# Kernel tuning notes

Hardware: AMD Instinct MI355X
Metric: run time of the kernel (lower is better)

The kernel has to match this reference:

```python
import jax, jax.numpy as jnp
import numpy as np

C_IN, C = 16, 32
N = 150000
SHAPE = (480, 360, 32)
SLOPE = 0.01  # LeakyReLU default
EPS = 1e-5    # BatchNorm1d default

# offset index into the canonical 27-neighbor table, ordered (dz, dy, dx)
P133 = tuple(9 + (dy + 1) * 3 + (dx + 1) for dy in (-1, 0, 1) for dx in (-1, 0, 1))   # kernel (1,3,3)
P313 = tuple((dz + 1) * 9 + 3 + (dx + 1) for dz in (-1, 0, 1) for dx in (-1, 0, 1))   # kernel (3,1,3)
P311 = tuple((dz + 1) * 9 + 4 for dz in (-1, 0, 1))                                   # kernel (3,1,1)
P131 = tuple(9 + (dy + 1) * 3 + 1 for dy in (-1, 0, 1))                               # kernel (1,3,1)
P113 = (12, 13, 14)                                                                   # kernel (1,1,3)


def setup_inputs() -> dict:
    rng = np.random.default_rng(0)
    # unique active voxel linear coords, sorted for searchsorted lookup
    lin = np.sort(rng.choice(SHAPE[0] * SHAPE[1] * SHAPE[2], size=N, replace=False))
    z, yx = np.divmod(lin, SHAPE[1] * SHAPE[2])
    y, x = np.divmod(yx, SHAPE[2])
    coords = np.stack([z, y, x], 1)  # [N,3]
    offs = np.array([[dz, dy, dx] for dz in (-1, 0, 1) for dy in (-1, 0, 1) for dx in (-1, 0, 1)])
    nc = coords[None] + offs[:, None]  # [27,N,3]
    valid = (nc >= 0).all(-1) & (nc[..., 0] < SHAPE[0]) & (nc[..., 1] < SHAPE[1]) & (nc[..., 2] < SHAPE[2])
    nlin = nc[..., 0] * SHAPE[1] * SHAPE[2] + nc[..., 1] * SHAPE[2] + nc[..., 2]
    pos = np.clip(np.searchsorted(lin, nlin), 0, N - 1)
    found = valid & (lin[pos] == nlin)
    nbr = np.where(found, pos, -1).astype(np.int32)  # [27,N], spconv indice pairs

    key = jax.random.key(0)
    ks = jax.random.split(key, 9)
    w = lambda k, kk, ci, co: jax.random.normal(k, (kk, ci, co), jnp.float32) * (1.0 / np.sqrt(kk * ci))
    bn_params = jnp.stack([
        jnp.stack([1.0 + 0.1 * jax.random.normal(jax.random.fold_in(ks[8], 4 * i + 0), (C,)),
                   0.1 * jax.random.normal(jax.random.fold_in(ks[8], 4 * i + 1), (C,)),
                   0.1 * jax.random.normal(jax.random.fold_in(ks[8], 4 * i + 2), (C,)),
                   0.5 + jax.random.uniform(jax.random.fold_in(ks[8], 4 * i + 3), (C,))])
        for i in range(7)
    ])  # [7,4,C]: gamma, beta, running_mean, running_var
    return {
        "x_feat": jax.random.normal(ks[0], (N, C_IN), jnp.float32),
        "nbr": jnp.asarray(nbr),
        "W1": w(ks[1], 9, C_IN, C), "W12": w(ks[2], 9, C, C),
        "W2": w(ks[3], 9, C_IN, C), "W3": w(ks[4], 9, C, C),
        "Wr1": w(ks[5], 3, C, C), "Wr2": w(ks[6], 3, C, C), "Wr3": w(ks[7], 3, C, C),
        "bn_params": bn_params,
    }


def _subm(feat, nbr, W, offs):
    """Submanifold sparse conv: gather -> masked GEMM -> same active set."""
    idx = nbr[jnp.asarray(offs)]              # [K,N]
    g = feat[jnp.clip(idx, 0)]                # [K,N,Cin]
    g = jnp.where((idx >= 0)[..., None], g, jnp.zeros((), feat.dtype))
    return jnp.einsum('knc,kcd->nd', g, W)    # [N,Cout]


def _bn(f, p):  # eval-mode BatchNorm1d
    gamma, beta, mean, var = p[0], p[1], p[2], p[3]
    return gamma * (f - mean) * jax.lax.rsqrt(var + EPS) + beta


def _lrelu(f):
    return jnp.where(f >= 0, f, SLOPE * f)


def reference(x_feat, nbr, W1, W12, W2, W3, Wr1, Wr2, Wr3, bn_params):
    # ResContextBlock (downCntx): act then BN, per source
    s = _bn(_lrelu(_subm(x_feat, nbr, W1, P133)), bn_params[0])
    s = _bn(_lrelu(_subm(s, nbr, W12, P313)), bn_params[1])
    r = _bn(_lrelu(_subm(x_feat, nbr, W2, P313)), bn_params[2])
    r = _bn(_lrelu(_subm(r, nbr, W3, P133)), bn_params[3])
    y = r + s
    # ReconBlock: three axial convs -> BN -> sigmoid, summed, gating multiply
    a = jax.nn.sigmoid(_bn(_subm(y, nbr, Wr1, P311), bn_params[4]))
    b = jax.nn.sigmoid(_bn(_subm(y, nbr, Wr2, P131), bn_params[5]))
    c = jax.nn.sigmoid(_bn(_subm(y, nbr, Wr3, P113), bn_params[6]))
    return (a + b + c) * y
```

## Files before the change

### kernel.cpp

```cpp
#include <hip/hip_runtime.h>
#include <cstdint>
#include <cstddef>


#define SLOPE 0.01f
#define BN_EPS 1e-5f

typedef __attribute__((ext_vector_type(8))) short bf16x8;
typedef __attribute__((ext_vector_type(4))) float f32x4;

__device__ __forceinline__ float bflo(uint32_t w) {
    union { uint32_t i; float f; } v; v.i = w << 16; return v.f;
}
__device__ __forceinline__ float bfhi(uint32_t w) {
    union { uint32_t i; float f; } v; v.i = w & 0xffff0000u; return v.f;
}
__device__ __forceinline__ float bf2f(uint16_t u) {
    union { uint32_t i; float f; } v; v.i = ((uint32_t)u) << 16; return v.f;
}
__device__ __forceinline__ uint16_t f2bf(float f) {
    union { float f; uint32_t i; } v; v.f = f;
    uint32_t x = v.i;
    return (uint16_t)((x + 0x7fffu + ((x >> 16) & 1u)) >> 16);
}

struct Taps9 { int t[9]; };
struct WSrcs { const void* p[8]; };

#define WFS     18432
#define WF_END  (5 * WFS)
#define BN_CNT  896

__device__ __forceinline__ int detect_f32_inline(const uint16_t* x16)
{
    int lane = threadIdx.x & 63;
    float a = bf2f(x16[4 * lane]);
    float b = bf2f(x16[4 * lane + 2]);
    int bad = (!(a > -16.f && a < 16.f)) || (!(b > -16.f && b < 16.f));
    return __ballot(bad) != 0ull;
}

__device__ __forceinline__ float readw(const void* p, int j, int f32)
{
    return f32 ? ((const float*)p)[j] : bf2f(((const uint16_t*)p)[j]);
}

__global__ void prep_all(const uint16_t* __restrict__ xprobe, WSrcs srcs,
                         uint16_t* __restrict__ Wf, float* __restrict__ bnf)
{
    int f32 = detect_f32_inline(xprobe);
    int i = blockIdx.x * 256 + threadIdx.x;
    if (i < WF_END) {
        int s = i / WFS, r = i - s * WFS;
        int t = r >> 11, T = (r >> 10) & 1;
        int co = (r >> 5) & 31, k = r & 31;
        uint16_t outv;
        if (s == 0 || s == 2) {
            int c = k >> 1, p = k & 1;
            float w = readw(srcs.p[s == 0 ? 0 : 2], (t * 16 + c) * 32 + co, f32);
            uint16_t h = f2bf(w);
            outv = (T == 0) ? h : (p == 0 ? f2bf(w - bf2f(h)) : (uint16_t)0);
        } else {
            float w;
            if (s == 4) {
                int g = t / 3, kk = t - g * 3;
                const void* bnp = srcs.p[7];
                float ga = readw(bnp, (4 + g) * 128 + co, f32);
                float va = readw(bnp, (4 + g) * 128 + 96 + co, f32);
                float scl = ga * rsqrtf(va + BN_EPS);
                w = readw(srcs.p[4 + g], (kk * 32 + k) * 32 + co, f32) * scl;
            } else {
                w = readw(srcs.p[s == 1 ? 1 : 3], (t * 32 + k) * 32 + co, f32);
            }
            uint16_t h = f2bf(w);
            outv = (T == 0) ? h : f2bf(w - bf2f(h));
        }
        Wf[i] = outv;
    } else if (i < WF_END + BN_CNT) {
        bnf[i - WF_END] = readw(srcs.p[7], i - WF_END, f32);
    }
}

__global__ void canon_x3(const void* __restrict__ xsrc,
                         uint32_t* __restrict__ xi, int total)
{
    int f32 = detect_f32_inline((const uint16_t*)xsrc);
    for (int i = blockIdx.x * blockDim.x + threadIdx.x; i < total;
         i += gridDim.x * blockDim.x) {
        float v = f32 ? ((const float*)xsrc)[i]
                      : bf2f(((const uint16_t*)xsrc)[i]);
        int row = i >> 4, c = i & 15;
        uint16_t h = f2bf(v);
        uint16_t l = f2bf(v - bf2f(h));
        xi[(size_t)row * 16 + c] = (uint32_t)h | ((uint32_t)l << 16);
    }
}

struct ConvJob {
    const uint16_t* feat;
    const uint16_t* Wf;
    const float*    bn;
    const uint16_t* addsrc;
    uint16_t*       out;
    Taps9 taps;
};

#define MFMA_BF16(A, B, C) __builtin_amdgcn_mfma_f32_16x16x32_bf16(A, B, C, 0, 0, 0)

__launch_bounds__(256, 3)
__global__ void conv_mfma5(ConvJob j0, ConvJob j1,
                           const int* __restrict__ nbr, int N)
{
    const ConvJob J = (blockIdx.y == 1) ? j1 : j0;
    const int tid = threadIdx.x;
    const int n0  = blockIdx.x * 128;
    const int lane = tid & 63;
    const int m = lane & 15, q = lane >> 4;
    const int vt0 = (tid >> 6) * 32;
    const bf16x8 Z8 = {0, 0, 0, 0, 0, 0, 0, 0};

    int rows[9][2];
#pragma unroll
    for (int t = 0; t < 9; ++t)
#pragma unroll
        for (int vt = 0; vt < 2; ++vt) {
            int n = n0 + vt0 + vt * 16 + m;
            rows[t][vt] = (n < N) ? nbr[(size_t)J.taps.t[t] * N + n] : -1;
        }
    __builtin_amdgcn_sched_barrier(0);

    bf16x8 A[9][2];
#pragma unroll
    for (int t = 0; t < 9; ++t)
#pragma unroll
        for (int vt = 0; vt < 2; ++vt) {
            int row = rows[t][vt];
            A[t][vt] = Z8;
            if (row >= 0)
                A[t][vt] = *(const bf16x8*)(J.feat + (size_t)row * 32 + q * 8);
        }
    __builtin_amdgcn_sched_barrier(0);

    f32x4 acc[2][2];
#pragma unroll
    for (int vt = 0; vt < 2; ++vt)
#pragma unroll
        for (int ot = 0; ot < 2; ++ot) acc[vt][ot] = {0.f, 0.f, 0.f, 0.f};

#pragma unroll
    for (int t = 0; t < 9; ++t) {
        const uint16_t* wb = J.Wf + t * 2048 + m * 32 + q * 8;
        bf16x8 B00 = *(const bf16x8*)(wb);
        bf16x8 B10 = *(const bf16x8*)(wb + 1024);
        bf16x8 B01 = *(const bf16x8*)(wb + 512);
        bf16x8 B11 = *(const bf16x8*)(wb + 1536);
#pragma unroll
        for (int vt = 0; vt < 2; ++vt) {
            acc[vt][0] = MFMA_BF16(A[t][vt], B00, acc[vt][0]);
            acc[vt][0] = MFMA_BF16(A[t][vt], B10, acc[vt][0]);
            acc[vt][1] = MFMA_BF16(A[t][vt], B01, acc[vt][1]);
            acc[vt][1] = MFMA_BF16(A[t][vt], B11, acc[vt][1]);
        }
    }

#pragma unroll
    for (int ot = 0; ot < 2; ++ot) {
        int ch = ot * 16 + m;
        float ga = J.bn[ch], be = J.bn[32 + ch];
        float mu = J.bn[64 + ch], va = J.bn[96 + ch];
        float s = ga * rsqrtf(va + BN_EPS);
        float b = be - mu * s;
#pragma unroll
        for (int vt = 0; vt < 2; ++vt)
#pragma unroll
            for (int r = 0; r < 4; ++r) {
                int vox = n0 + vt0 + vt * 16 + q * 4 + r;
                if (vox >= N) continue;
                float xv = acc[vt][ot][r];
                xv = (xv >= 0.f) ? xv : SLOPE * xv;
                float o = xv * s + b;
                if (J.addsrc) o += bf2f(J.addsrc[(size_t)vox * 32 + ch]);
                J.out[(size_t)vox * 32 + ch] = f2bf(o);
            }
    }
}

__launch_bounds__(256, 3)
__global__ void recon_mfma5(const uint16_t* __restrict__ y16,
                            const uint16_t* __restrict__ xprobe,
                            const int* __restrict__ nbr,
                            const uint16_t* __restrict__ Wf4,
                            const float* __restrict__ bnf,
                            void* __restrict__ out_, int N)
{
    const int out_f32 = detect_f32_inline(xprobe);
    const int tid = threadIdx.x;
    const int n0  = blockIdx.x * 128;
    const int lane = tid & 63;
    const int m = lane & 15, q = lane >> 4;
    const int vt0 = (tid >> 6) * 32;
    const bf16x8 Z8 = {0, 0, 0, 0, 0, 0, 0, 0};

    const int ut[7] = {4, 22, 10, 16, 12, 14, 13};
    int rows[7][2];
#pragma unroll
    for (int t = 0; t < 7; ++t)
#pragma unroll
        for (int vt = 0; vt < 2; ++vt) {
            int n = n0 + vt0 + vt * 16 + m;
            rows[t][vt] = (n < N) ? nbr[(size_t)ut[t] * N + n] : -1;
        }
    __builtin_amdgcn_sched_barrier(0);

    bf16x8 A[7][2];
#pragma unroll
    for (int t = 0; t < 7; ++t)
#pragma unroll
        for (int vt = 0; vt < 2; ++vt) {
            int row = rows[t][vt];
            A[t][vt] = Z8;
            if (row >= 0)
                A[t][vt] = *(const bf16x8*)(y16 + (size_t)row * 32 + q * 8);
        }
    __builtin_amdgcn_sched_barrier(0);

    f32x4 a[3][2][2];
#pragma unroll
    for (int g = 0; g < 3; ++g)
#pragma unroll
        for (int vt = 0; vt < 2; ++vt)
#pragma unroll
            for (int ot = 0; ot < 2; ++ot) a[g][vt][ot] = {0.f, 0.f, 0.f, 0.f};

#pragma unroll
    for (int e = 0; e < 3; ++e)
#pragma unroll
        for (int s2 = 0; s2 < 2; ++s2) {
            int slot = 2 * e + s2;
            int t = e * 3 + s2 * 2;
            const uint16_t* wb = Wf4 + t * 2048 + m * 32 + q * 8;
            bf16x8 B00 = *(const bf16x8*)(wb);
            bf16x8 B10 = *(const bf16x8*)(wb + 1024);
            bf16x8 B01 = *(const bf16x8*)(wb + 512);
            bf16x8 B11 = *(const bf16x8*)(wb + 1536);
#pragma unroll
            for (int vt = 0; vt < 2; ++vt) {
                a[e][vt][0] = MFMA_BF16(A[slot][vt], B00, a[e][vt][0]);
                a[e][vt][0] = MFMA_BF16(A[slot][vt], B10, a[e][vt][0]);
                a[e][vt][1] = MFMA_BF16(A[slot][vt], B01, a[e][vt][1]);
                a[e][vt][1] = MFMA_BF16(A[slot][vt], B11, a[e][vt][1]);
            }
        }
#pragma unroll
    for (int g = 0; g < 3; ++g) {
        const uint16_t* wb = Wf4 + (g * 3 + 1) * 2048 + m * 32 + q * 8;
        bf16x8 B00 = *(const bf16x8*)(wb);
        bf16x8 B10 = *(const bf16x8*)(wb + 1024);
        bf16x8 B01 = *(const bf16x8*)(wb + 512);
        bf16x8 B11 = *(const bf16x8*)(wb + 1536);
#pragma unroll
        for (int vt = 0; vt < 2; ++vt) {
            a[g][vt][0] = MFMA_BF16(A[6][vt], B00, a[g][vt][0]);
            a[g][vt][0] = MFMA_BF16(A[6][vt], B10, a[g][vt][0]);
            a[g][vt][1] = MFMA_BF16(A[6][vt], B01, a[g][vt][1]);
            a[g][vt][1] = MFMA_BF16(A[6][vt], B11, a[g][vt][1]);
        }
    }

#pragma unroll
    for (int ot = 0; ot < 2; ++ot) {
        int ch = ot * 16 + m;
        float sh[3];
#pragma unroll
        for (int g = 0; g < 3; ++g) {
            const float* p = bnf + (size_t)(4 + g) * 128;
            float scl = p[ch] * rsqrtf(p[96 + ch] + BN_EPS);
            sh[g] = p[32 + ch] - p[64 + ch] * scl;
        }
#pragma unroll
        for (int vt = 0; vt < 2; ++vt)
#pragma unroll
            for (int r = 0; r < 4; ++r) {
                int vox = n0 + vt0 + vt * 16 + q * 4 + r;
                if (vox >= N) continue;
                float g0 = 1.f / (1.f + __expf(-(a[0][vt][ot][r] + sh[0])));
                float g1 = 1.f / (1.f + __expf(-(a[1][vt][ot][r] + sh[1])));
                float g2 = 1.f / (1.f + __expf(-(a[2][vt][ot][r] + sh[2])));
                float o = (g0 + g1 + g2) * bf2f(y16[(size_t)vox * 32 + ch]);
                if (out_f32)
                    ((float*)out_)[(size_t)vox * 32 + ch] = o;
                else
                    ((uint16_t*)out_)[(size_t)vox * 32 + ch] = f2bf(o);
            }
    }
}

#define WC_W1   0
#define WC_W12  4608
#define WC_W2   13824
#define WC_W3   18432
#define WC_WR1  27648
#define WC_WR2  30720
#define WC_WR3  33792
#define WC_BNP  36864
#define WC_END  37760

__global__ void canon_weights_fb(WSrcs srcs, float* __restrict__ Wc,
                                 const uint16_t* __restrict__ xprobe)
{
    int f32 = detect_f32_inline(xprobe);
    const int offs[9] = {WC_W1, WC_W12, WC_W2, WC_W3, WC_WR1, WC_WR2,
                         WC_WR3, WC_BNP, WC_END};
    int i = blockIdx.x * 256 + threadIdx.x;
    if (i >= WC_END) return;
    int t = 0;
#pragma unroll
    for (int k = 1; k < 8; ++k) if (i >= offs[k]) t = k;
    Wc[i] = readw(srcs.p[t], i - offs[t], f32);
}

__global__ void canon_x_bf(const void* __restrict__ xsrc,
                           uint16_t* __restrict__ xc, int n)
{
    int f32 = detect_f32_inline((const uint16_t*)xsrc);
    for (int i = blockIdx.x * blockDim.x + threadIdx.x; i < n;
         i += gridDim.x * blockDim.x) {
        float v = f32 ? ((const float*)xsrc)[i]
                      : bf2f(((const uint16_t*)xsrc)[i]);
        xc[i] = f2bf(v);
    }
}

template<int CIN>
__launch_bounds__(256)
__global__ void conv_bn_lrelu_bf(const uint16_t* __restrict__ feat,
                                 const int* __restrict__ nbr,
                                 const float* __restrict__ Wg,
                                 const float* __restrict__ bnp,
                                 const uint16_t* __restrict__ addsrc,
                                 uint16_t* __restrict__ out,
                                 Taps9 taps, int N)
{
    __shared__ float Wl[9 * CIN * 32];
    __shared__ float fs[CIN][128];
    __shared__ int   sidx[128];
    __shared__ float bns[32], bnb[32];

    const int tid = threadIdx.x;
    const int n0  = blockIdx.x * 128;

    for (int i = tid; i < 9 * CIN * 32; i += 256) Wl[i] = Wg[i];
    if (tid < 32) {
        float g = bnp[tid], b = bnp[32 + tid];
        float mu = bnp[64 + tid], va = bnp[96 + tid];
        float s = g * rsqrtf(va + BN_EPS);
        bns[tid] = s; bnb[tid] = b - mu * s;
    }
    float acc[4][4];
#pragma unroll
    for (int v = 0; v < 4; ++v)
#pragma unroll
        for (int j = 0; j < 4; ++j) acc[v][j] = 0.f;

    const int vb = (tid >> 3) << 2, cg = (tid & 7) << 2;
    const int r = tid >> 1, h = tid & 1, j0 = h * (CIN / 2);

#pragma unroll 1
    for (int t = 0; t < 9; ++t) {
        __syncthreads();
        if (tid < 128) {
            int n = n0 + tid;
            sidx[tid] = (n < N) ? nbr[(size_t)taps.t[t] * N + n] : -1;
        }
        __syncthreads();
        int mm = sidx[r];
        if (mm >= 0) {
            const uint16_t* src = feat + (size_t)mm * CIN + j0;
#pragma unroll
            for (int qq = 0; qq < CIN / 2; qq += 8) {
                uint4 u = *reinterpret_cast<const uint4*>(src + qq);
                fs[j0 + qq + 0][r] = bflo(u.x); fs[j0 + qq + 1][r] = bfhi(u.x);
                fs[j0 + qq + 2][r] = bflo(u.y); fs[j0 + qq + 3][r] = bfhi(u.y);
                fs[j0 + qq + 4][r] = bflo(u.z); fs[j0 + qq + 5][r] = bfhi(u.z);
                fs[j0 + qq + 6][r] = bflo(u.w); fs[j0 + qq + 7][r] = bfhi(u.w);
            }
        } else {
#pragma unroll
            for (int qq = 0; qq < CIN / 2; ++qq) fs[j0 + qq][r] = 0.f;
        }
        __syncthreads();
        const float* wk = Wl + t * (CIN * 32) + cg;
#pragma unroll
        for (int ci = 0; ci < CIN; ++ci) {
            float4 f = *reinterpret_cast<const float4*>(&fs[ci][vb]);
            float4 w = *reinterpret_cast<const float4*>(wk + ci * 32);
            acc[0][0] += f.x * w.x; acc[0][1] += f.x * w.y; acc[0][2] += f.x * w.z; acc[0][3] += f.x * w.w;
            acc[1][0] += f.y * w.x; acc[1][1] += f.y * w.y; acc[1][2] += f.y * w.z; acc[1][3] += f.y * w.w;
            acc[2][0] += f.z * w.x; acc[2][1] += f.z * w.y; acc[2][2] += f.z * w.z; acc[2][3] += f.z * w.w;
            acc[3][0] += f.w * w.x; acc[3][1] += f.w * w.y; acc[3][2] += f.w * w.z; acc[3][3] += f.w * w.w;
        }
    }
#pragma unroll
    for (int v = 0; v < 4; ++v) {
        int n = n0 + vb + v;
        if (n >= N) continue;
        ushort4 st;
        uint16_t* ov = (uint16_t*)&st;
#pragma unroll
        for (int j = 0; j < 4; ++j) {
            float x = acc[v][j];
            x = (x >= 0.f) ? x : SLOPE * x;
            float o = x * bns[cg + j] + bnb[cg + j];
            if (addsrc) o += bf2f(addsrc[(size_t)n * 32 + cg + j]);
            ov[j] = f2bf(o);
        }
        *reinterpret_cast<ushort4*>(out + (size_t)n * 32 + cg) = st;
    }
}

__launch_bounds__(256, 4)
__global__ void recon_gate_bf(const uint16_t* __restrict__ y,
                              const int* __restrict__ nbr,
                              const float* __restrict__ Wc,
                              const uint16_t* __restrict__ xprobe,
                              void* __restrict__ out_, int N)
{
    __shared__ float Wl[3 * 32 * 32];
    __shared__ float fs[32][128];
    __shared__ int   sidx[128];
    __shared__ float scl[3][32], shf[3][32];

    const int tid = threadIdx.x;
    const int n0  = blockIdx.x * 128;
    const int out_f32 = detect_f32_inline(xprobe);

    if (tid < 96) {
        int g = tid >> 5, c = tid & 31;
        const float* p = Wc + WC_BNP + (size_t)(4 + g) * 128;
        float ga = p[c], be = p[32 + c], mu = p[64 + c], va = p[96 + c];
        float s = ga * rsqrtf(va + BN_EPS);
        scl[g][c] = s; shf[g][c] = be - mu * s;
    }
    const int vb = (tid >> 3) << 2, cg = (tid & 7) << 2;
    const int r = tid >> 1, h = tid & 1, j0 = h * 16;

    float gsum[4][4];
#pragma unroll
    for (int v = 0; v < 4; ++v)
#pragma unroll
        for (int j = 0; j < 4; ++j) gsum[v][j] = 0.f;

    const int taps[3][3] = {{4, 13, 22}, {10, 13, 16}, {12, 13, 14}};

#pragma unroll 1
    for (int g = 0; g < 3; ++g) {
        __syncthreads();
        {
            const float* src = Wc + WC_WR1 + g * 3072;
            for (int i = tid; i < 3072; i += 256)
                Wl[i] = src[i] * scl[g][i & 31];
        }
        float acc[4][4];
#pragma unroll
        for (int v = 0; v < 4; ++v)
#pragma unroll
            for (int j = 0; j < 4; ++j) acc[v][j] = 0.f;

#pragma unroll 1
        for (int k = 0; k < 3; ++k) {
            __syncthreads();
            if (tid < 128) {
                int n = n0 + tid;
                sidx[tid] = (n < N) ? nbr[(size_t)taps[g][k] * N + n] : -1;
            }
            __syncthreads();
            int mm = sidx[r];
            if (mm >= 0) {
                const uint16_t* src = y + (size_t)mm * 32 + j0;
#pragma unroll
                for (int qq = 0; qq < 16; qq += 8) {
                    uint4 u = *reinterpret_cast<const uint4*>(src + qq);
                    fs[j0 + qq + 0][r] = bflo(u.x); fs[j0 + qq + 1][r] = bfhi(u.x);
                    fs[j0 + qq + 2][r] = bflo(u.y); fs[j0 + qq + 3][r] = bfhi(u.y);
                    fs[j0 + qq + 4][r] = bflo(u.z); fs[j0 + qq + 5][r] = bfhi(u.z);
                    fs[j0 + qq + 6][r] = bflo(u.w); fs[j0 + qq + 7][r] = bfhi(u.w);
                }
            } else {
#pragma unroll
                for (int qq = 0; qq < 16; ++qq) fs[j0 + qq][r] = 0.f;
            }
            __syncthreads();
            const float* wk = Wl + k * (32 * 32) + cg;
#pragma unroll
            for (int ci = 0; ci < 32; ++ci) {
                float4 f = *reinterpret_cast<const float4*>(&fs[ci][vb]);
                float4 w = *reinterpret_cast<const float4*>(wk + ci * 32);
                acc[0][0] += f.x * w.x; acc[0][1] += f.x * w.y; acc[0][2] += f.x * w.z; acc[0][3] += f.x * w.w;
                acc[1][0] += f.y * w.x; acc[1][1] += f.y * w.y; acc[1][2] += f.y * w.z; acc[1][3] += f.y * w.w;
                acc[2][0] += f.z * w.x; acc[2][1] += f.z * w.y; acc[2][2] += f.z * w.z; acc[2][3] += f.z * w.w;
                acc[3][0] += f.w * w.x; acc[3][1] += f.w * w.y; acc[3][2] += f.w * w.z; acc[3][3] += f.w * w.w;
            }
        }
#pragma unroll
        for (int v = 0; v < 4; ++v)
#pragma unroll
            for (int j = 0; j < 4; ++j) {
                float x = acc[v][j] + shf[g][cg + j];
                gsum[v][j] += 1.f / (1.f + __expf(-x));
            }
    }
#pragma unroll
    for (int v = 0; v < 4; ++v) {
        int n = n0 + vb + v;
        if (n >= N) continue;
#pragma unroll
        for (int j = 0; j < 4; ++j) {
            float yv = bf2f(y[(size_t)n * 32 + cg + j]);
            float o = gsum[v][j] * yv;
            if (out_f32) ((float*)out_)[(size_t)n * 32 + cg + j] = o;
            else ((uint16_t*)out_)[(size_t)n * 32 + cg + j] = f2bf(o);
        }
    }
}

extern "C" void kernel_launch(void* const* d_in, const int* in_sizes, int n_in,
                              void* d_out, int out_size, void* d_ws, size_t ws_size,
                              hipStream_t stream)
{
    (void)n_in; (void)out_size;
    const void* x   = d_in[0];
    const int*  nbr = (const int*)d_in[1];
    const int N = in_sizes[0] / 16;
    const uint16_t* xprobe = (const uint16_t*)x;

    dim3 block(256);
    const int gx = (N + 127) / 128;
    Taps9 p133 = {{9, 10, 11, 12, 13, 14, 15, 16, 17}};
    Taps9 p313 = {{3, 4, 5, 12, 13, 14, 21, 22, 23}};
    WSrcs ws8 = {{ d_in[2], d_in[3], d_in[4], d_in[5],
                   d_in[6], d_in[7], d_in[8], d_in[9] }};

    float*    bnf = (float*)d_ws;
    uint16_t* Wf  = (uint16_t*)((char*)d_ws + 4096);
    const size_t base2 = 4096u + (size_t)WF_END * 2;
    uint16_t* xi  = (uint16_t*)((char*)d_ws + base2);
    uint16_t* A1  = xi + (size_t)N * 32;
    uint16_t* A2  = A1 + (size_t)N * 32;
    uint16_t* B1  = A2 + (size_t)N * 32;
    const size_t need = base2 + 4u * (size_t)N * 64;

    if (ws_size >= need) {
        prep_all<<<(WF_END + BN_CNT + 255) / 256, block, 0, stream>>>(xprobe, ws8, Wf, bnf);
        canon_x3<<<1024, block, 0, stream>>>(x, (uint32_t*)xi, N * 16);
        ConvJob c1  = {xi, Wf + 0 * WFS, bnf + 0 * 128, nullptr, A1, p133};
        ConvJob c2  = {xi, Wf + 2 * WFS, bnf + 2 * 128, nullptr, A2, p313};
        ConvJob c12 = {A1, Wf + 1 * WFS, bnf + 1 * 128, nullptr, B1, p313};
        ConvJob c3  = {A2, Wf + 3 * WFS, bnf + 3 * 128, B1,      A1, p133};
        conv_mfma5<<<dim3(gx, 2), block, 0, stream>>>(c1, c2, nbr, N);
        conv_mfma5<<<dim3(gx, 1), block, 0, stream>>>(c12, c12, nbr, N);
        conv_mfma5<<<dim3(gx, 1), block, 0, stream>>>(c3, c3, nbr, N);
        recon_mfma5<<<gx, block, 0, stream>>>(A1, xprobe, nbr, Wf + 4 * WFS, bnf, d_out, N);
    } else {
        float*    Wc = (float*)d_ws;
        uint16_t* xc = (uint16_t*)((char*)d_ws + (size_t)WC_END * 4 + 256);
        uint16_t* A  = (uint16_t*)d_out;
        uint16_t* B  = xc + (size_t)N * 16;
        const float* bn0 = Wc + WC_BNP + 0 * 128;
        const float* bn1 = Wc + WC_BNP + 1 * 128;
        const float* bn2 = Wc + WC_BNP + 2 * 128;
        const float* bn3 = Wc + WC_BNP + 3 * 128;
        canon_weights_fb<<<(WC_END + 255) / 256, block, 0, stream>>>(ws8, Wc, xprobe);
        canon_x_bf<<<1024, block, 0, stream>>>(x, xc, N * 16);
        conv_bn_lrelu_bf<16><<<gx, block, 0, stream>>>(xc, nbr, Wc + WC_W1,  bn0, nullptr, A, p133, N);
        conv_bn_lrelu_bf<32><<<gx, block, 0, stream>>>(A,  nbr, Wc + WC_W12, bn1, nullptr, B, p313, N);
        conv_bn_lrelu_bf<16><<<gx, block, 0, stream>>>(xc, nbr, Wc + WC_W2,  bn2, nullptr, A, p313, N);
        conv_bn_lrelu_bf<32><<<gx, block, 0, stream>>>(A,  nbr, Wc + WC_W3,  bn3, B,       B, p133, N);
        recon_gate_bf<<<gx, block, 0, stream>>>(B, nbr, Wc, xprobe, d_out, N);
    }
}
```

Before: 195.0 us.

## Skip empty neighbor taps per wave and stage gathers in groups for occupancy

Uses a wave ballot to find taps where no voxel in a 16-row tile has a neighbor, and skips the feature gather, weight loads and MFMAs for those taps. Gathers are split into three groups of taps instead of loading all 9 (or 7) up front, which cuts live registers, and launch bounds go from 3 to 4 blocks per CU. The recon kernel also folds each axial branch's sigmoid into a running sum right away, so three accumulator sets no longer stay live. The cost is less memory-level parallelism, since fewer gathers are in flight before the MFMAs start, plus some divergence-free branching overhead.

```diff
diff --git a/kernel.cpp b/kernel.cpp
--- a/kernel.cpp
+++ b/kernel.cpp
@@ -107,8 +107,8 @@
 
 #define MFMA_BF16(A, B, C) __builtin_amdgcn_mfma_f32_16x16x32_bf16(A, B, C, 0, 0, 0)
 
-__launch_bounds__(256, 3)
-__global__ void conv_mfma5(ConvJob j0, ConvJob j1,
+__launch_bounds__(256, 4)
+__global__ void conv_mfma6(ConvJob j0, ConvJob j1,
                            const int* __restrict__ nbr, int N)
 {
     const ConvJob J = (blockIdx.y == 1) ? j1 : j0;
@@ -129,17 +129,12 @@
         }
     __builtin_amdgcn_sched_barrier(0);
 
-    bf16x8 A[9][2];
+    bool act[9][2];
 #pragma unroll
     for (int t = 0; t < 9; ++t)
 #pragma unroll
-        for (int vt = 0; vt < 2; ++vt) {
-            int row = rows[t][vt];
-            A[t][vt] = Z8;
-            if (row >= 0)
-                A[t][vt] = *(const bf16x8*)(J.feat + (size_t)row * 32 + q * 8);
-        }
-    __builtin_amdgcn_sched_barrier(0);
+        for (int vt = 0; vt < 2; ++vt)
+            act[t][vt] = __ballot(rows[t][vt] >= 0) != 0ull;
 
     f32x4 acc[2][2];
 #pragma unroll
@@ -148,18 +143,39 @@
         for (int ot = 0; ot < 2; ++ot) acc[vt][ot] = {0.f, 0.f, 0.f, 0.f};
 
 #pragma unroll
-    for (int t = 0; t < 9; ++t) {
-        const uint16_t* wb = J.Wf + t * 2048 + m * 32 + q * 8;
-        bf16x8 B00 = *(const bf16x8*)(wb);
-        bf16x8 B10 = *(const bf16x8*)(wb + 1024);
-        bf16x8 B01 = *(const bf16x8*)(wb + 512);
-        bf16x8 B11 = *(const bf16x8*)(wb + 1536);
-#pragma unroll
-        for (int vt = 0; vt < 2; ++vt) {
-            acc[vt][0] = MFMA_BF16(A[t][vt], B00, acc[vt][0]);
-            acc[vt][0] = MFMA_BF16(A[t][vt], B10, acc[vt][0]);
-            acc[vt][1] = MFMA_BF16(A[t][vt], B01, acc[vt][1]);
-            acc[vt][1] = MFMA_BF16(A[t][vt], B11, acc[vt][1]);
+    for (int g = 0; g < 3; ++g) {
+        bf16x8 A[3][2];
+#pragma unroll
+        for (int i = 0; i < 3; ++i)
+#pragma unroll
+            for (int vt = 0; vt < 2; ++vt) {
+                const int t = g * 3 + i;
+                A[i][vt] = Z8;
+                if (act[t][vt]) {
+                    int row = rows[t][vt];
+                    if (row >= 0)
+                        A[i][vt] = *(const bf16x8*)(J.feat + (size_t)row * 32 + q * 8);
+                }
+            }
+        __builtin_amdgcn_sched_barrier(0);
+
+#pragma unroll
+        for (int i = 0; i < 3; ++i) {
+            const int t = g * 3 + i;
+            if (!(act[t][0] || act[t][1])) continue;
+            const uint16_t* wb = J.Wf + t * 2048 + m * 32 + q * 8;
+            bf16x8 B00 = *(const bf16x8*)(wb);
+            bf16x8 B10 = *(const bf16x8*)(wb + 1024);
+            bf16x8 B01 = *(const bf16x8*)(wb + 512);
+            bf16x8 B11 = *(const bf16x8*)(wb + 1536);
+#pragma unroll
+            for (int vt = 0; vt < 2; ++vt) {
+                if (!act[t][vt]) continue;
+                acc[vt][0] = MFMA_BF16(A[i][vt], B00, acc[vt][0]);
+                acc[vt][0] = MFMA_BF16(A[i][vt], B10, acc[vt][0]);
+                acc[vt][1] = MFMA_BF16(A[i][vt], B01, acc[vt][1]);
+                acc[vt][1] = MFMA_BF16(A[i][vt], B11, acc[vt][1]);
+            }
         }
     }
 
@@ -185,8 +201,8 @@
     }
 }
 
-__launch_bounds__(256, 3)
-__global__ void recon_mfma5(const uint16_t* __restrict__ y16,
+__launch_bounds__(256, 4)
+__global__ void recon_mfma6(const uint16_t* __restrict__ y16,
                             const uint16_t* __restrict__ xprobe,
                             const int* __restrict__ nbr,
                             const uint16_t* __restrict__ Wf4,
@@ -212,32 +228,58 @@
         }
     __builtin_amdgcn_sched_barrier(0);
 
-    bf16x8 A[7][2];
+    bool act[7][2];
 #pragma unroll
     for (int t = 0; t < 7; ++t)
 #pragma unroll
-        for (int vt = 0; vt < 2; ++vt) {
-            int row = rows[t][vt];
-            A[t][vt] = Z8;
-            if (row >= 0)
-                A[t][vt] = *(const bf16x8*)(y16 + (size_t)row * 32 + q * 8);
-        }
-    __builtin_amdgcn_sched_barrier(0);
-
-    f32x4 a[3][2][2];
-#pragma unroll
-    for (int g = 0; g < 3; ++g)
-#pragma unroll
         for (int vt = 0; vt < 2; ++vt)
-#pragma unroll
-            for (int ot = 0; ot < 2; ++ot) a[g][vt][ot] = {0.f, 0.f, 0.f, 0.f};
-
-#pragma unroll
-    for (int e = 0; e < 3; ++e)
+            act[t][vt] = __ballot(rows[t][vt] >= 0) != 0ull;
+
+    bf16x8 A6[2];
+#pragma unroll
+    for (int vt = 0; vt < 2; ++vt) {
+        int row = rows[6][vt];
+        A6[vt] = Z8;
+        if (row >= 0)
+            A6[vt] = *(const bf16x8*)(y16 + (size_t)row * 32 + q * 8);
+    }
+
+    float gsum[2][2][4];
+#pragma unroll
+    for (int vt = 0; vt < 2; ++vt)
+#pragma unroll
+        for (int ot = 0; ot < 2; ++ot)
+#pragma unroll
+            for (int r = 0; r < 4; ++r) gsum[vt][ot][r] = 0.f;
+
+#pragma unroll
+    for (int g = 0; g < 3; ++g) {
+        f32x4 acc[2][2];
+#pragma unroll
+        for (int vt = 0; vt < 2; ++vt)
+#pragma unroll
+            for (int ot = 0; ot < 2; ++ot) acc[vt][ot] = {0.f, 0.f, 0.f, 0.f};
+
+        bf16x8 Ae[2][2];
+#pragma unroll
+        for (int s2 = 0; s2 < 2; ++s2)
+#pragma unroll
+            for (int vt = 0; vt < 2; ++vt) {
+                const int slot = 2 * g + s2;
+                Ae[s2][vt] = Z8;
+                if (act[slot][vt]) {
+                    int row = rows[slot][vt];
+                    if (row >= 0)
+                        Ae[s2][vt] = *(const bf16x8*)(y16 + (size_t)row * 32 + q * 8);
+                }
+            }
+        __builtin_amdgcn_sched_barrier(0);
+
 #pragma unroll
         for (int s2 = 0; s2 < 2; ++s2) {
-            int slot = 2 * e + s2;
-            int t = e * 3 + s2 * 2;
+            const int slot = 2 * g + s2;
+            if (!(act[slot][0] || act[slot][1])) continue;
+            const int t = g * 3 + s2 * 2;
             const uint16_t* wb = Wf4 + t * 2048 + m * 32 + q * 8;
             bf16x8 B00 = *(const bf16x8*)(wb);
             bf16x8 B10 = *(const bf16x8*)(wb + 1024);
@@ -245,48 +287,53 @@
             bf16x8 B11 = *(const bf16x8*)(wb + 1536);
 #pragma unroll
             for (int vt = 0; vt < 2; ++vt) {
-                a[e][vt][0] = MFMA_BF16(A[slot][vt], B00, a[e][vt][0]);
-                a[e][vt][0] = MFMA_BF16(A[slot][vt], B10, a[e][vt][0]);
-                a[e][vt][1] = MFMA_BF16(A[slot][vt], B01, a[e][vt][1]);
-                a[e][vt][1] = MFMA_BF16(A[slot][vt], B11, a[e][vt][1]);
-            }
-        }
-#pragma unroll
-    for (int g = 0; g < 3; ++g) {
-        const uint16_t* wb = Wf4 + (g * 3 + 1) * 2048 + m * 32 + q * 8;
-        bf16x8 B00 = *(const bf16x8*)(wb);
-        bf16x8 B10 = *(const bf16x8*)(wb + 1024);
-        bf16x8 B01 = *(const bf16x8*)(wb + 512);
-        bf16x8 B11 = *(const bf16x8*)(wb + 1536);
-#pragma unroll
-        for (int vt = 0; vt < 2; ++vt) {
-            a[g][vt][0] = MFMA_BF16(A[6][vt], B00, a[g][vt][0]);
-            a[g][vt][0] = MFMA_BF16(A[6][vt], B10, a[g][vt][0]);
-            a[g][vt][1] = MFMA_BF16(A[6][vt], B01, a[g][vt][1]);
-            a[g][vt][1] = MFMA_BF16(A[6][vt], B11, a[g][vt][1]);
+                if (!act[slot][vt]) continue;
+                acc[vt][0] = MFMA_BF16(Ae[s2][vt], B00, acc[vt][0]);
+                acc[vt][0] = MFMA_BF16(Ae[s2][vt], B10, acc[vt][0]);
+                acc[vt][1] = MFMA_BF16(Ae[s2][vt], B01, acc[vt][1]);
+                acc[vt][1] = MFMA_BF16(Ae[s2][vt], B11, acc[vt][1]);
+            }
+        }
+        {
+            const uint16_t* wb = Wf4 + (g * 3 + 1) * 2048 + m * 32 + q * 8;
+            bf16x8 B00 = *(const bf16x8*)(wb);
+            bf16x8 B10 = *(const bf16x8*)(wb + 1024);
+            bf16x8 B01 = *(const bf16x8*)(wb + 512);
+            bf16x8 B11 = *(const bf16x8*)(wb + 1536);
+#pragma unroll
+            for (int vt = 0; vt < 2; ++vt) {
+                acc[vt][0] = MFMA_BF16(A6[vt], B00, acc[vt][0]);
+                acc[vt][0] = MFMA_BF16(A6[vt], B10, acc[vt][0]);
+                acc[vt][1] = MFMA_BF16(A6[vt], B01, acc[vt][1]);
+                acc[vt][1] = MFMA_BF16(A6[vt], B11, acc[vt][1]);
+            }
+        }
+
+#pragma unroll
+        for (int ot = 0; ot < 2; ++ot) {
+            int ch = ot * 16 + m;
+            const float* p = bnf + (size_t)(4 + g) * 128;
+            float scl = p[ch] * rsqrtf(p[96 + ch] + BN_EPS);
+            float sh = p[32 + ch] - p[64 + ch] * scl;
+#pragma unroll
+            for (int vt = 0; vt < 2; ++vt)
+#pragma unroll
+                for (int r = 0; r < 4; ++r)
+                    gsum[vt][ot][r] +=
+                        1.f / (1.f + __expf(-(acc[vt][ot][r] + sh)));
         }
     }
 
 #pragma unroll
     for (int ot = 0; ot < 2; ++ot) {
         int ch = ot * 16 + m;
-        float sh[3];
-#pragma unroll
-        for (int g = 0; g < 3; ++g) {
-            const float* p = bnf + (size_t)(4 + g) * 128;
-            float scl = p[ch] * rsqrtf(p[96 + ch] + BN_EPS);
-            sh[g] = p[32 + ch] - p[64 + ch] * scl;
-        }
 #pragma unroll
         for (int vt = 0; vt < 2; ++vt)
 #pragma unroll
             for (int r = 0; r < 4; ++r) {
                 int vox = n0 + vt0 + vt * 16 + q * 4 + r;
                 if (vox >= N) continue;
-                float g0 = 1.f / (1.f + __expf(-(a[0][vt][ot][r] + sh[0])));
-                float g1 = 1.f / (1.f + __expf(-(a[1][vt][ot][r] + sh[1])));
-                float g2 = 1.f / (1.f + __expf(-(a[2][vt][ot][r] + sh[2])));
-                float o = (g0 + g1 + g2) * bf2f(y16[(size_t)vox * 32 + ch]);
+                float o = gsum[vt][ot][r] * bf2f(y16[(size_t)vox * 32 + ch]);
                 if (out_f32)
                     ((float*)out_)[(size_t)vox * 32 + ch] = o;
                 else
@@ -556,10 +603,10 @@
         ConvJob c2  = {xi, Wf + 2 * WFS, bnf + 2 * 128, nullptr, A2, p313};
         ConvJob c12 = {A1, Wf + 1 * WFS, bnf + 1 * 128, nullptr, B1, p313};
         ConvJob c3  = {A2, Wf + 3 * WFS, bnf + 3 * 128, B1,      A1, p133};
-        conv_mfma5<<<dim3(gx, 2), block, 0, stream>>>(c1, c2, nbr, N);
-        conv_mfma5<<<dim3(gx, 1), block, 0, stream>>>(c12, c12, nbr, N);
-        conv_mfma5<<<dim3(gx, 1), block, 0, stream>>>(c3, c3, nbr, N);
-        recon_mfma5<<<gx, block, 0, stream>>>(A1, xprobe, nbr, Wf + 4 * WFS, bnf, d_out, N);
+        conv_mfma6<<<dim3(gx, 2), block, 0, stream>>>(c1, c2, nbr, N);
+        conv_mfma6<<<dim3(gx, 1), block, 0, stream>>>(c12, c12, nbr, N);
+        conv_mfma6<<<dim3(gx, 1), block, 0, stream>>>(c3, c3, nbr, N);
+        recon_mfma6<<<gx, block, 0, stream>>>(A1, xprobe, nbr, Wf + 4 * WFS, bnf, d_out, N);
     } else {
         float*    Wc = (float*)d_ws;
         uint16_t* xc = (uint16_t*)((char*)d_ws + (size_t)WC_END * 4 + 256);
```

Measured after the change: 170.7 us. 12.5% less time.
